# Optimization experiments

Measured on AMD Instinct MI355X. Metric: run time of the kernel, lower is better.

## Reference

```python
import jax, jax.numpy as jnp
import numpy as np

X1_DIM = 256
X2_DIM = 128
HIDDEN = 256
N = 1024


def _init_linear(key, fan_in, fan_out):
    kw, kb = jax.random.split(key)
    bound = 1.0 / np.sqrt(fan_in)
    W = jax.random.uniform(kw, (fan_in, fan_out), jnp.float32, -bound, bound)
    b = jax.random.uniform(kb, (fan_out,), jnp.float32, -bound, bound)
    return W, b


def setup_inputs() -> dict:
    key = jax.random.key(0)
    k1, k2, k3, k4, k5 = jax.random.split(key, 5)
    x1 = jax.random.normal(k1, (N, X1_DIM), jnp.float32)
    x2 = jax.random.normal(k2, (N, X2_DIM), jnp.float32)
    W1, b1 = _init_linear(k3, X1_DIM, HIDDEN)
    W2, b2 = _init_linear(k4, HIDDEN, HIDDEN)
    W3, b3 = _init_linear(k5, HIDDEN, 2 * X2_DIM)
    return {"x1": x1, "x2": x2, "W1": W1, "b1": b1, "W2": W2, "b2": b2, "W3": W3, "b3": b3}


def reference(x1, x2, W1, b1, W2, b2, W3, b3):
    # gaussian MLP: Linear -> ReLU -> Linear -> ReLU -> Linear -> Tanh
    h = jax.nn.relu(x1 @ W1 + b1)
    h = jax.nn.relu(h @ W2 + b2)
    g = jnp.tanh(h @ W3 + b3)                    # [N, 2*D]
    mu, logvar = jnp.split(g, 2, axis=-1)        # each [N, D]
    inv_var = jnp.exp(-logvar)                   # [N, D]
    # positive term: per-sample conditional log-likelihood
    pos = -0.5 * (mu - x2) ** 2 * inv_var        # [N, D]
    # negative term: pairwise broadcast [N, N, D] then mean over the j axis
    diff2 = (mu[:, None, :] - x2[None, :, :]) ** 2   # [N, N, D]
    neg = -0.5 * diff2.mean(axis=1) * inv_var        # [N, D]
    mi_ub = (pos.sum(axis=-1) - neg.sum(axis=-1)).mean()
    return mi_ub
```

## Files before the change

kernel.cpp:

```cpp
#include <hip/hip_runtime.h>

#define NR 1024
#define ROWS 4
#define NBLK (NR / ROWS)
#define NTHR 1024

__global__ __launch_bounds__(256) void stats_kernel(const float* __restrict__ x2,
                                                    float* __restrict__ ws,
                                                    float* __restrict__ out) {
    int tid = threadIdx.x;
    int d = tid & 127;
    int g = tid >> 7;
    int row0 = blockIdx.x * 128 + g;
    float s = 0.f, s2 = 0.f;
#pragma unroll 8
    for (int i = 0; i < 64; i++) {
        float v = x2[(row0 + 2 * i) * 128 + d];
        s += v;
        s2 += v * v;
    }
    __shared__ float sh[256];
    __shared__ float sh2[256];
    sh[tid] = s;
    sh2[tid] = s2;
    __syncthreads();
    if (g == 0) {
        ws[blockIdx.x * 256 + d]       = sh[tid] + sh[tid + 128];
        ws[blockIdx.x * 256 + 128 + d] = sh2[tid] + sh2[tid + 128];
    }
    if (blockIdx.x == 0 && tid == 0) out[0] = 0.f;
}

__device__ __forceinline__ void layer(const float* __restrict__ in_lds,
                                      const float* __restrict__ W,
                                      const float* __restrict__ b,
                                      float* __restrict__ out_lds,
                                      float* __restrict__ red,
                                      int tid, int c, int h, int act) {
    const float* Wp = W + c;
    const float4* in4 = (const float4*)in_lds;
    float a0 = 0.f, a1 = 0.f, a2 = 0.f, a3 = 0.f;
    int kb = h * 64;
#pragma unroll
    for (int s = 0; s < 16; s++) {
        int k = kb + s * 4;
        float w0 = Wp[(k + 0) * 256];
        float w1 = Wp[(k + 1) * 256];
        float w2 = Wp[(k + 2) * 256];
        float w3 = Wp[(k + 3) * 256];
        float4 xa = in4[0 * 64 + (k >> 2)];
        float4 xb = in4[1 * 64 + (k >> 2)];
        float4 xc = in4[2 * 64 + (k >> 2)];
        float4 xd = in4[3 * 64 + (k >> 2)];
        a0 = fmaf(xa.x, w0, a0); a0 = fmaf(xa.y, w1, a0); a0 = fmaf(xa.z, w2, a0); a0 = fmaf(xa.w, w3, a0);
        a1 = fmaf(xb.x, w0, a1); a1 = fmaf(xb.y, w1, a1); a1 = fmaf(xb.z, w2, a1); a1 = fmaf(xb.w, w3, a1);
        a2 = fmaf(xc.x, w0, a2); a2 = fmaf(xc.y, w1, a2); a2 = fmaf(xc.z, w2, a2); a2 = fmaf(xc.w, w3, a2);
        a3 = fmaf(xd.x, w0, a3); a3 = fmaf(xd.y, w1, a3); a3 = fmaf(xd.z, w2, a3); a3 = fmaf(xd.w, w3, a3);
    }
    float4 v; v.x = a0; v.y = a1; v.z = a2; v.w = a3;
    ((float4*)red)[tid] = v;
    __syncthreads();
    if (h == 0) {
        float bias = b[c];
        float4 s0 = ((float4*)red)[c];
        float4 s1 = ((float4*)red)[c + 256];
        float4 s2 = ((float4*)red)[c + 512];
        float4 s3 = ((float4*)red)[c + 768];
        float r0 = bias + s0.x + s1.x + s2.x + s3.x;
        float r1 = bias + s0.y + s1.y + s2.y + s3.y;
        float r2 = bias + s0.z + s1.z + s2.z + s3.z;
        float r3 = bias + s0.w + s1.w + s2.w + s3.w;
        if (act == 0) {
            r0 = fmaxf(r0, 0.f); r1 = fmaxf(r1, 0.f);
            r2 = fmaxf(r2, 0.f); r3 = fmaxf(r3, 0.f);
        } else {
            r0 = tanhf(r0); r1 = tanhf(r1); r2 = tanhf(r2); r3 = tanhf(r3);
        }
        out_lds[0 * 256 + c] = r0;
        out_lds[1 * 256 + c] = r1;
        out_lds[2 * 256 + c] = r2;
        out_lds[3 * 256 + c] = r3;
    }
    __syncthreads();
}

__global__ __launch_bounds__(1024, 4) void club_kernel(
    const float* __restrict__ x1, const float* __restrict__ x2,
    const float* __restrict__ W1, const float* __restrict__ b1,
    const float* __restrict__ W2, const float* __restrict__ b2,
    const float* __restrict__ W3, const float* __restrict__ b3,
    const float* __restrict__ part, float* __restrict__ out) {
    __shared__ float bufA[ROWS * 256];
    __shared__ float bufB[ROWS * 256];
    __shared__ float x2s[ROWS * 128];
    __shared__ float stat[256];
    __shared__ float red[NTHR * 4];
    __shared__ double dred[16];

    int tid = threadIdx.x;
    int c = tid & 255;
    int h = tid >> 8;
    int row0 = blockIdx.x * ROWS;

    if (tid < 256) {
        ((float4*)bufA)[tid] = ((const float4*)(x1 + row0 * 256))[tid];
    } else if (tid < 384) {
        ((float4*)x2s)[tid - 256] = ((const float4*)(x2 + row0 * 128))[tid - 256];
    } else if (tid >= 512 && tid < 768) {
        int t = tid - 512;
        float s = 0.f;
#pragma unroll
        for (int p = 0; p < 8; p++) s += part[p * 256 + t];
        stat[t] = s * (1.f / 1024.f);
    }
    __syncthreads();

    layer(bufA, W1, b1, bufB, red, tid, c, h, 0);
    layer(bufB, W2, b2, bufA, red, tid, c, h, 0);
    layer(bufA, W3, b3, bufB, red, tid, c, h, 1);

    double p = 0.0;
    if (tid < 512) {
        int d = tid & 127;
        int r = tid >> 7;
        double mu = (double)bufB[r * 256 + d];
        double lv = (double)bufB[r * 256 + 128 + d];
        double xv = (double)x2s[r * 128 + d];
        double mx = (double)stat[d];
        double mxsq = (double)stat[128 + d];
        double iv = exp(-lv);
        p = -0.5 * iv * (xv * xv - mxsq - 2.0 * mu * (xv - mx));
    }
#pragma unroll
    for (int off = 32; off > 0; off >>= 1) p += __shfl_down(p, off, 64);
    int lane = tid & 63, wv = tid >> 6;
    if (lane == 0) dred[wv] = p;
    __syncthreads();
    if (tid == 0) {
        double s = 0.0;
#pragma unroll
        for (int i = 0; i < 16; i++) s += dred[i];
        atomicAdd(out, (float)(s * (1.0 / 1024.0)));
    }
}

extern "C" void kernel_launch(void* const* d_in, const int* in_sizes, int n_in,
                              void* d_out, int out_size, void* d_ws, size_t ws_size,
                              hipStream_t stream) {
    const float* x1 = (const float*)d_in[0];
    const float* x2 = (const float*)d_in[1];
    const float* W1 = (const float*)d_in[2];
    const float* b1 = (const float*)d_in[3];
    const float* W2 = (const float*)d_in[4];
    const float* b2 = (const float*)d_in[5];
    const float* W3 = (const float*)d_in[6];
    const float* b3 = (const float*)d_in[7];
    float* out = (float*)d_out;
    float* ws = (float*)d_ws;

    stats_kernel<<<8, 256, 0, stream>>>(x2, ws, out);
    club_kernel<<<NBLK, NTHR, 0, stream>>>(x1, x2, W1, b1, W2, b2, W3, b3, ws, out);
}
```

Before: 91.29 us.

## Register-tile MLP layers 4x4 and reduce K-split partials with DPP/swizzle

```diff
diff --git a/kernel.cpp b/kernel.cpp
--- a/kernel.cpp
+++ b/kernel.cpp
@@ -4,6 +4,19 @@
 #define ROWS 4
 #define NBLK (NR / ROWS)
 #define NTHR 1024
+
+__device__ __forceinline__ float xor1v(float v) {
+    return __int_as_float(__builtin_amdgcn_mov_dpp(__float_as_int(v), 0xB1, 0xF, 0xF, true));
+}
+__device__ __forceinline__ float xor2v(float v) {
+    return __int_as_float(__builtin_amdgcn_mov_dpp(__float_as_int(v), 0x4E, 0xF, 0xF, true));
+}
+__device__ __forceinline__ float xor4v(float v) {
+    return __int_as_float(__builtin_amdgcn_ds_swizzle(__float_as_int(v), 0x101F));
+}
+__device__ __forceinline__ float xor8v(float v) {
+    return __int_as_float(__builtin_amdgcn_ds_swizzle(__float_as_int(v), 0x201F));
+}
 
 __global__ __launch_bounds__(256) void stats_kernel(const float* __restrict__ x2,
                                                     float* __restrict__ ws,
@@ -35,52 +48,66 @@
                                       const float* __restrict__ W,
                                       const float* __restrict__ b,
                                       float* __restrict__ out_lds,
-                                      float* __restrict__ red,
-                                      int tid, int c, int h, int act) {
-    const float* Wp = W + c;
+                                      int h, int c4, int act) {
+    float acc[16];
+#pragma unroll
+    for (int t = 0; t < 16; t++) acc[t] = 0.f;
     const float4* in4 = (const float4*)in_lds;
-    float a0 = 0.f, a1 = 0.f, a2 = 0.f, a3 = 0.f;
-    int kb = h * 64;
 #pragma unroll
-    for (int s = 0; s < 16; s++) {
-        int k = kb + s * 4;
-        float w0 = Wp[(k + 0) * 256];
-        float w1 = Wp[(k + 1) * 256];
-        float w2 = Wp[(k + 2) * 256];
-        float w3 = Wp[(k + 3) * 256];
-        float4 xa = in4[0 * 64 + (k >> 2)];
-        float4 xb = in4[1 * 64 + (k >> 2)];
-        float4 xc = in4[2 * 64 + (k >> 2)];
-        float4 xd = in4[3 * 64 + (k >> 2)];
-        a0 = fmaf(xa.x, w0, a0); a0 = fmaf(xa.y, w1, a0); a0 = fmaf(xa.z, w2, a0); a0 = fmaf(xa.w, w3, a0);
-        a1 = fmaf(xb.x, w0, a1); a1 = fmaf(xb.y, w1, a1); a1 = fmaf(xb.z, w2, a1); a1 = fmaf(xb.w, w3, a1);
-        a2 = fmaf(xc.x, w0, a2); a2 = fmaf(xc.y, w1, a2); a2 = fmaf(xc.z, w2, a2); a2 = fmaf(xc.w, w3, a2);
-        a3 = fmaf(xd.x, w0, a3); a3 = fmaf(xd.y, w1, a3); a3 = fmaf(xd.z, w2, a3); a3 = fmaf(xd.w, w3, a3);
+    for (int j = 0; j < 4; j++) {
+        int k0 = h * 4 + j * 64;
+        float4 w[4];
+        w[0] = *(const float4*)(W + (k0 + 0) * 256 + c4);
+        w[1] = *(const float4*)(W + (k0 + 1) * 256 + c4);
+        w[2] = *(const float4*)(W + (k0 + 2) * 256 + c4);
+        w[3] = *(const float4*)(W + (k0 + 3) * 256 + c4);
+        float4 xr[4];
+        xr[0] = in4[0 * 64 + h + j * 16];
+        xr[1] = in4[1 * 64 + h + j * 16];
+        xr[2] = in4[2 * 64 + h + j * 16];
+        xr[3] = in4[3 * 64 + h + j * 16];
+#pragma unroll
+        for (int r = 0; r < 4; r++) {
+#pragma unroll
+            for (int c = 0; c < 4; c++) {
+                float a = acc[r * 4 + c];
+                a = fmaf(((const float*)&xr[r])[0], ((const float*)&w[0])[c], a);
+                a = fmaf(((const float*)&xr[r])[1], ((const float*)&w[1])[c], a);
+                a = fmaf(((const float*)&xr[r])[2], ((const float*)&w[2])[c], a);
+                a = fmaf(((const float*)&xr[r])[3], ((const float*)&w[3])[c], a);
+                acc[r * 4 + c] = a;
+            }
+        }
     }
-    float4 v; v.x = a0; v.y = a1; v.z = a2; v.w = a3;
-    ((float4*)red)[tid] = v;
-    __syncthreads();
-    if (h == 0) {
-        float bias = b[c];
-        float4 s0 = ((float4*)red)[c];
-        float4 s1 = ((float4*)red)[c + 256];
-        float4 s2 = ((float4*)red)[c + 512];
-        float4 s3 = ((float4*)red)[c + 768];
-        float r0 = bias + s0.x + s1.x + s2.x + s3.x;
-        float r1 = bias + s0.y + s1.y + s2.y + s3.y;
-        float r2 = bias + s0.z + s1.z + s2.z + s3.z;
-        float r3 = bias + s0.w + s1.w + s2.w + s3.w;
-        if (act == 0) {
-            r0 = fmaxf(r0, 0.f); r1 = fmaxf(r1, 0.f);
-            r2 = fmaxf(r2, 0.f); r3 = fmaxf(r3, 0.f);
-        } else {
-            r0 = tanhf(r0); r1 = tanhf(r1); r2 = tanhf(r2); r3 = tanhf(r3);
-        }
-        out_lds[0 * 256 + c] = r0;
-        out_lds[1 * 256 + c] = r1;
-        out_lds[2 * 256 + c] = r2;
-        out_lds[3 * 256 + c] = r3;
+    float r8[8];
+#pragma unroll
+    for (int t = 0; t < 8; t++) {
+        float lo = acc[t] + xor1v(acc[t]);
+        float hi = acc[t + 8] + xor1v(acc[t + 8]);
+        r8[t] = (h & 1) ? hi : lo;
     }
+    float r4[4];
+#pragma unroll
+    for (int t = 0; t < 4; t++) {
+        float lo = r8[t] + xor2v(r8[t]);
+        float hi = r8[t + 4] + xor2v(r8[t + 4]);
+        r4[t] = (h & 2) ? hi : lo;
+    }
+    float r2[2];
+#pragma unroll
+    for (int t = 0; t < 2; t++) {
+        float lo = r4[t] + xor4v(r4[t]);
+        float hi = r4[t + 2] + xor4v(r4[t + 2]);
+        r2[t] = (h & 4) ? hi : lo;
+    }
+    float lo = r2[0] + xor8v(r2[0]);
+    float hi = r2[1] + xor8v(r2[1]);
+    float sum = (h & 8) ? hi : lo;
+    int r_out = ((h & 1) << 1) | ((h >> 1) & 1);
+    int c_out = (((h >> 2) & 1) << 1) | ((h >> 3) & 1);
+    float v = sum + b[c4 + c_out];
+    v = act ? tanhf(v) : fmaxf(v, 0.f);
+    out_lds[r_out * 256 + c4 + c_out] = v;
     __syncthreads();
 }
 
@@ -94,12 +121,12 @@
     __shared__ float bufB[ROWS * 256];
     __shared__ float x2s[ROWS * 128];
     __shared__ float stat[256];
-    __shared__ float red[NTHR * 4];
     __shared__ double dred[16];
 
     int tid = threadIdx.x;
-    int c = tid & 255;
-    int h = tid >> 8;
+    int lane = tid & 63, wv = tid >> 6;
+    int h = lane & 15;
+    int c4 = (wv * 4 + (lane >> 4)) * 4;
     int row0 = blockIdx.x * ROWS;
 
     if (tid < 256) {
@@ -115,9 +142,9 @@
     }
     __syncthreads();
 
-    layer(bufA, W1, b1, bufB, red, tid, c, h, 0);
-    layer(bufB, W2, b2, bufA, red, tid, c, h, 0);
-    layer(bufA, W3, b3, bufB, red, tid, c, h, 1);
+    layer(bufA, W1, b1, bufB, h, c4, 0);
+    layer(bufB, W2, b2, bufA, h, c4, 0);
+    layer(bufA, W3, b3, bufB, h, c4, 1);
 
     double p = 0.0;
     if (tid < 512) {
@@ -133,7 +160,6 @@
     }
 #pragma unroll
     for (int off = 32; off > 0; off >>= 1) p += __shfl_down(p, off, 64);
-    int lane = tid & 63, wv = tid >> 6;
     if (lane == 0) dred[wv] = p;
     __syncthreads();
     if (tid == 0) {
```

Result: slower. 99.41 us (+8.9%).

## Remap MLP layer threads to two columns each with eight-way K split and widen stats grid

Applied to the files above, without the earlier changes.

```diff
diff --git a/kernel.cpp b/kernel.cpp
--- a/kernel.cpp
+++ b/kernel.cpp
@@ -2,8 +2,9 @@
 
 #define NR 1024
 #define ROWS 4
-#define NBLK (NR / ROWS)
+#define NBLK 256
 #define NTHR 1024
+#define SBLK 32
 
 __global__ __launch_bounds__(256) void stats_kernel(const float* __restrict__ x2,
                                                     float* __restrict__ ws,
@@ -11,16 +12,15 @@
     int tid = threadIdx.x;
     int d = tid & 127;
     int g = tid >> 7;
-    int row0 = blockIdx.x * 128 + g;
+    int row0 = blockIdx.x * 32 + g;
     float s = 0.f, s2 = 0.f;
-#pragma unroll 8
-    for (int i = 0; i < 64; i++) {
+#pragma unroll
+    for (int i = 0; i < 16; i++) {
         float v = x2[(row0 + 2 * i) * 128 + d];
         s += v;
         s2 += v * v;
     }
-    __shared__ float sh[256];
-    __shared__ float sh2[256];
+    __shared__ float sh[256], sh2[256];
     sh[tid] = s;
     sh2[tid] = s2;
     __syncthreads();
@@ -36,51 +36,52 @@
                                       const float* __restrict__ b,
                                       float* __restrict__ out_lds,
                                       float* __restrict__ red,
-                                      int tid, int c, int h, int act) {
-    const float* Wp = W + c;
+                                      int g, int q, int act) {
+    float acc[8];
+#pragma unroll
+    for (int e = 0; e < 8; e++) acc[e] = 0.f;
     const float4* in4 = (const float4*)in_lds;
-    float a0 = 0.f, a1 = 0.f, a2 = 0.f, a3 = 0.f;
-    int kb = h * 64;
+    const float2* Wp = (const float2*)W + g;
+    int k0 = q * 32;
 #pragma unroll
-    for (int s = 0; s < 16; s++) {
-        int k = kb + s * 4;
-        float w0 = Wp[(k + 0) * 256];
-        float w1 = Wp[(k + 1) * 256];
-        float w2 = Wp[(k + 2) * 256];
-        float w3 = Wp[(k + 3) * 256];
-        float4 xa = in4[0 * 64 + (k >> 2)];
-        float4 xb = in4[1 * 64 + (k >> 2)];
-        float4 xc = in4[2 * 64 + (k >> 2)];
-        float4 xd = in4[3 * 64 + (k >> 2)];
-        a0 = fmaf(xa.x, w0, a0); a0 = fmaf(xa.y, w1, a0); a0 = fmaf(xa.z, w2, a0); a0 = fmaf(xa.w, w3, a0);
-        a1 = fmaf(xb.x, w0, a1); a1 = fmaf(xb.y, w1, a1); a1 = fmaf(xb.z, w2, a1); a1 = fmaf(xb.w, w3, a1);
-        a2 = fmaf(xc.x, w0, a2); a2 = fmaf(xc.y, w1, a2); a2 = fmaf(xc.z, w2, a2); a2 = fmaf(xc.w, w3, a2);
-        a3 = fmaf(xd.x, w0, a3); a3 = fmaf(xd.y, w1, a3); a3 = fmaf(xd.z, w2, a3); a3 = fmaf(xd.w, w3, a3);
+    for (int j = 0; j < 8; j++) {
+        int k = k0 + 4 * j;
+        float2 w0 = Wp[(k + 0) * 128];
+        float2 w1 = Wp[(k + 1) * 128];
+        float2 w2 = Wp[(k + 2) * 128];
+        float2 w3 = Wp[(k + 3) * 128];
+        float4 xa = in4[0 * 64 + 8 * q + j];
+        float4 xb = in4[1 * 64 + 8 * q + j];
+        float4 xc = in4[2 * 64 + 8 * q + j];
+        float4 xd = in4[3 * 64 + 8 * q + j];
+        acc[0] = fmaf(xa.x, w0.x, acc[0]); acc[1] = fmaf(xa.x, w0.y, acc[1]);
+        acc[0] = fmaf(xa.y, w1.x, acc[0]); acc[1] = fmaf(xa.y, w1.y, acc[1]);
+        acc[0] = fmaf(xa.z, w2.x, acc[0]); acc[1] = fmaf(xa.z, w2.y, acc[1]);
+        acc[0] = fmaf(xa.w, w3.x, acc[0]); acc[1] = fmaf(xa.w, w3.y, acc[1]);
+        acc[2] = fmaf(xb.x, w0.x, acc[2]); acc[3] = fmaf(xb.x, w0.y, acc[3]);
+        acc[2] = fmaf(xb.y, w1.x, acc[2]); acc[3] = fmaf(xb.y, w1.y, acc[3]);
+        acc[2] = fmaf(xb.z, w2.x, acc[2]); acc[3] = fmaf(xb.z, w2.y, acc[3]);
+        acc[2] = fmaf(xb.w, w3.x, acc[2]); acc[3] = fmaf(xb.w, w3.y, acc[3]);
+        acc[4] = fmaf(xc.x, w0.x, acc[4]); acc[5] = fmaf(xc.x, w0.y, acc[5]);
+        acc[4] = fmaf(xc.y, w1.x, acc[4]); acc[5] = fmaf(xc.y, w1.y, acc[5]);
+        acc[4] = fmaf(xc.z, w2.x, acc[4]); acc[5] = fmaf(xc.z, w2.y, acc[5]);
+        acc[4] = fmaf(xc.w, w3.x, acc[4]); acc[5] = fmaf(xc.w, w3.y, acc[5]);
+        acc[6] = fmaf(xd.x, w0.x, acc[6]); acc[7] = fmaf(xd.x, w0.y, acc[7]);
+        acc[6] = fmaf(xd.y, w1.x, acc[6]); acc[7] = fmaf(xd.y, w1.y, acc[7]);
+        acc[6] = fmaf(xd.z, w2.x, acc[6]); acc[7] = fmaf(xd.z, w2.y, acc[7]);
+        acc[6] = fmaf(xd.w, w3.x, acc[6]); acc[7] = fmaf(xd.w, w3.y, acc[7]);
     }
-    float4 v; v.x = a0; v.y = a1; v.z = a2; v.w = a3;
-    ((float4*)red)[tid] = v;
+#pragma unroll
+    for (int e = 0; e < 8; e++) red[q * 1024 + e * 128 + g] = acc[e];
     __syncthreads();
-    if (h == 0) {
-        float bias = b[c];
-        float4 s0 = ((float4*)red)[c];
-        float4 s1 = ((float4*)red)[c + 256];
-        float4 s2 = ((float4*)red)[c + 512];
-        float4 s3 = ((float4*)red)[c + 768];
-        float r0 = bias + s0.x + s1.x + s2.x + s3.x;
-        float r1 = bias + s0.y + s1.y + s2.y + s3.y;
-        float r2 = bias + s0.z + s1.z + s2.z + s3.z;
-        float r3 = bias + s0.w + s1.w + s2.w + s3.w;
-        if (act == 0) {
-            r0 = fmaxf(r0, 0.f); r1 = fmaxf(r1, 0.f);
-            r2 = fmaxf(r2, 0.f); r3 = fmaxf(r3, 0.f);
-        } else {
-            r0 = tanhf(r0); r1 = tanhf(r1); r2 = tanhf(r2); r3 = tanhf(r3);
-        }
-        out_lds[0 * 256 + c] = r0;
-        out_lds[1 * 256 + c] = r1;
-        out_lds[2 * 256 + c] = r2;
-        out_lds[3 * 256 + c] = r3;
-    }
+    float s = 0.f;
+#pragma unroll
+    for (int q2 = 0; q2 < 8; q2++) s += red[q2 * 1024 + q * 128 + g];
+    int r = q >> 1;
+    int col = 2 * g + (q & 1);
+    float v = s + b[col];
+    v = act ? tanhf(v) : fmaxf(v, 0.f);
+    out_lds[r * 256 + col] = v;
     __syncthreads();
 }
 
@@ -94,12 +95,13 @@
     __shared__ float bufB[ROWS * 256];
     __shared__ float x2s[ROWS * 128];
     __shared__ float stat[256];
-    __shared__ float red[NTHR * 4];
+    __shared__ float red[8 * 8 * 128];
     __shared__ double dred[16];
 
     int tid = threadIdx.x;
-    int c = tid & 255;
-    int h = tid >> 8;
+    int lane = tid & 63, wv = tid >> 6;
+    int g = tid & 127;
+    int q = tid >> 7;
     int row0 = blockIdx.x * ROWS;
 
     if (tid < 256) {
@@ -110,14 +112,14 @@
         int t = tid - 512;
         float s = 0.f;
 #pragma unroll
-        for (int p = 0; p < 8; p++) s += part[p * 256 + t];
+        for (int p = 0; p < SBLK; p++) s += part[p * 256 + t];
         stat[t] = s * (1.f / 1024.f);
     }
     __syncthreads();
 
-    layer(bufA, W1, b1, bufB, red, tid, c, h, 0);
-    layer(bufB, W2, b2, bufA, red, tid, c, h, 0);
-    layer(bufA, W3, b3, bufB, red, tid, c, h, 1);
+    layer(bufA, W1, b1, bufB, red, g, q, 0);
+    layer(bufB, W2, b2, bufA, red, g, q, 0);
+    layer(bufA, W3, b3, bufB, red, g, q, 1);
 
     double p = 0.0;
     if (tid < 512) {
@@ -133,7 +135,6 @@
     }
 #pragma unroll
     for (int off = 32; off > 0; off >>= 1) p += __shfl_down(p, off, 64);
-    int lane = tid & 63, wv = tid >> 6;
     if (lane == 0) dred[wv] = p;
     __syncthreads();
     if (tid == 0) {
@@ -158,6 +159,6 @@
     float* out = (float*)d_out;
     float* ws = (float*)d_ws;
 
-    stats_kernel<<<8, 256, 0, stream>>>(x2, ws, out);
+    stats_kernel<<<SBLK, 256, 0, stream>>>(x2, ws, out);
     club_kernel<<<NBLK, NTHR, 0, stream>>>(x1, x2, W1, b1, W2, b2, W3, b3, ws, out);
 }
```

New measurement: 86.02 us. 5.8% less time.
